# Optimization experiments

Measured on AMD Instinct MI355X. Metric: run time of the kernel, lower is better.

The kernel has to match this reference:

```python
import jax, jax.numpy as jnp
import numpy as np

B, S, HID = 2, 2048, 2048
H, D, KV = 16, 128, 4          # heads, head_dim, kv heads
REP = H // KV                  # GQA repeat factor
THETA = 10000.0


def setup_inputs() -> dict:
    key = jax.random.key(0)
    ks = jax.random.split(key, 12)
    query = jax.random.normal(ks[0], (B, S, HID), jnp.float32)
    k_in = jax.random.normal(ks[1], (B, S, HID), jnp.float32)
    v_in = jax.random.normal(ks[2], (B, S, HID), jnp.float32)
    # additive causal mask: 0 on/below diag, -10000 above
    causal = jnp.tril(jnp.ones((S, S), jnp.float32))
    mask = jnp.broadcast_to((1.0 - causal) * -10000.0, (B, 1, S, S))
    # rotary tables (cos/sin of freqs_cis), shape [S, D//2]
    inv_freq = 1.0 / (THETA ** (jnp.arange(0, D, 2, dtype=jnp.float32) / D))
    ang = jnp.outer(jnp.arange(S, dtype=jnp.float32), inv_freq)
    freqs_cos, freqs_sin = jnp.cos(ang), jnp.sin(ang)
    sd = 0.02
    Wq = jax.random.normal(ks[3], (HID, H * D), jnp.float32) * sd
    bq = jnp.zeros((H * D,), jnp.float32)
    Wk = jax.random.normal(ks[4], (HID, KV * D), jnp.float32) * sd
    bk = jnp.zeros((KV * D,), jnp.float32)
    Wv = jax.random.normal(ks[5], (HID, KV * D), jnp.float32) * sd
    bv = jnp.zeros((KV * D,), jnp.float32)
    Wo = jax.random.normal(ks[6], (H * D, HID), jnp.float32) * sd
    bo = jnp.zeros((HID,), jnp.float32)
    return {"query": query, "key": k_in, "value": v_in, "mask": mask,
            "freqs_cos": freqs_cos, "freqs_sin": freqs_sin,
            "Wq": Wq, "bq": bq, "Wk": Wk, "bk": bk,
            "Wv": Wv, "bv": bv, "Wo": Wo, "bo": bo}


def _rope(x, cos, sin):
    # x: [B,S,h,D]; pairs adjacent dims as complex (view_as_complex)
    xr = x.reshape(*x.shape[:-1], D // 2, 2)
    xe, xo = xr[..., 0], xr[..., 1]
    c = cos[None, :, None, :]
    s = sin[None, :, None, :]
    re = xe * c - xo * s
    im = xe * s + xo * c
    return jnp.stack([re, im], axis=-1).reshape(x.shape)


def reference(query, key, value, mask, freqs_cos, freqs_sin,
              Wq, bq, Wk, bk, Wv, bv, Wo, bo):
    q = (query @ Wq + bq).reshape(B, S, H, D)
    k = (key @ Wk + bk).reshape(B, S, KV, D)
    v = (value @ Wv + bv).reshape(B, S, KV, D)
    # repeat_kv: torch.repeat_interleave along head dim
    k = jnp.repeat(k, REP, axis=2)
    v = jnpp_repeat = jnp.repeat(v, REP, axis=2)
    q = _rope(q, freqs_cos, freqs_sin)
    k = _rope(k, freqs_cos, freqs_sin)
    q = q.transpose(0, 2, 1, 3)  # [B,H,S,D]
    k = k.transpose(0, 2, 1, 3)
    v = v.transpose(0, 2, 1, 3)
    scores = jnp.einsum('bhqd,bhkd->bhqk', q, k) / jnp.sqrt(jnp.float32(D))
    scores = scores + mask
    probs = jax.nn.softmax(scores, axis=-1)
    ctx = jnp.einsum('bhqk,bhkd->bhqd', probs, v)
    ctx = ctx.transpose(0, 2, 1, 3).reshape(B, S, H * D)
    return ctx @ Wo + bo
```

## Files before the change

kernel.cpp:

```cpp
#include <hip/hip_runtime.h>
#include <stdint.h>

#define BB 2
#define SS 2048
#define HID 2048
#define NH 16
#define DD 128
#define NKV 4

typedef unsigned short u16;
typedef __attribute__((ext_vector_type(8))) short short8;
typedef __attribute__((ext_vector_type(4))) float f32x4;

#if __has_builtin(__builtin_amdgcn_exp2f)
#define EXP2(x) __builtin_amdgcn_exp2f(x)
#else
#define EXP2(x) exp2f(x)
#endif

__device__ __forceinline__ u16 f2bf(float x) {
    union { float f; unsigned u; } v; v.f = x;
    unsigned u = v.u;
    return (u16)((u + 0x7FFFu + ((u >> 16) & 1u)) >> 16);
}

__device__ __forceinline__ void async_lds16(const void* g, void* l) {
    __builtin_amdgcn_global_load_lds(
        (const __attribute__((address_space(1))) void*)(uintptr_t)g,
        (__attribute__((address_space(3))) void*)(uintptr_t)l,
        16, 0, 0);
}

__global__ __launch_bounds__(256) void k_prep(const float* __restrict__ query,
                                              const float* __restrict__ key,
                                              const float* __restrict__ value,
                                              const float* __restrict__ Wq,
                                              const float* __restrict__ Wk,
                                              const float* __restrict__ Wv,
                                              const float* __restrict__ Wo,
                                              u16* __restrict__ qbf,
                                              u16* __restrict__ kbf,
                                              u16* __restrict__ vbf,
                                              u16* __restrict__ Wt,
                                              u16* __restrict__ Wot) {
    __shared__ float tile[32][33];
    int x = blockIdx.x;
    if (x < 24576) {
        const float* in; u16* out;
        if (x < 8192)       { in = query; out = qbf; }
        else if (x < 16384) { in = key;   out = kbf; x -= 8192; }
        else                { in = value; out = vbf; x -= 16384; }
        const int i = x * 256 + threadIdx.x;
        float4 v = ((const float4*)in)[i];
        uint2 o;
        o.x = (unsigned)f2bf(v.x) | ((unsigned)f2bf(v.y) << 16);
        o.y = (unsigned)f2bf(v.z) | ((unsigned)f2bf(v.w) << 16);
        ((uint2*)out)[i] = o;
        return;
    }
    const int v_ = x - 24576;
    const int ty = v_ / 160;
    const int xt = v_ - ty * 160;
    const float* src; u16* dst; int N, n0;
    if (xt < 64)      { src = Wq; dst = Wt;                          N = 2048; n0 = xt * 32; }
    else if (xt < 80) { src = Wk; dst = Wt + (size_t)2048 * 2048;    N = 512;  n0 = (xt - 64) * 32; }
    else if (xt < 96) { src = Wv; dst = Wt + (size_t)2560 * 2048;    N = 512;  n0 = (xt - 80) * 32; }
    else              { src = Wo; dst = Wot;                         N = 2048; n0 = (xt - 96) * 32; }
    const int k0 = ty * 32;
    const int c = threadIdx.x & 31, r = threadIdx.x >> 5;
#pragma unroll
    for (int i = 0; i < 32; i += 8)
        tile[r + i][c] = src[(size_t)(k0 + r + i) * N + n0 + c];
    __syncthreads();
#pragma unroll
    for (int i = 0; i < 32; i += 8)
        dst[(size_t)(n0 + r + i) * 2048 + k0 + c] = f2bf(tile[c][r + i]);
}

__global__ __launch_bounds__(256) void k_gemm_qkv(const u16* __restrict__ qbf,
                                                  const u16* __restrict__ kbf,
                                                  const u16* __restrict__ vbf,
                                                  const u16* __restrict__ Wt,
                                                  const float* __restrict__ bq,
                                                  const float* __restrict__ bk,
                                                  const float* __restrict__ bv,
                                                  const float* __restrict__ fc,
                                                  const float* __restrict__ fs,
                                                  u16* __restrict__ qro,
                                                  u16* __restrict__ kro,
                                                  u16* __restrict__ vtr) {
    __shared__ char smem[32768];
    u16* As = (u16*)smem;
    u16* Bs = (u16*)(smem + 16384);
    float* Ep = (float*)smem;

    const int tid = threadIdx.x;
    const int lane = tid & 63, wave = tid >> 6;
    const int bn = blockIdx.x;
    const int bm = blockIdx.y * 128;
    const u16* A = (bn < 16) ? qbf : (bn < 20) ? kbf : vbf;

    const int srow = wave * 8 + (lane >> 3);
    const int c0 = ((lane & 7) ^ (lane >> 3)) * 8;
    const u16* gA = A  + (size_t)(bm + srow) * 2048 + c0;
    const u16* gB = Wt + (size_t)(bn * 128 + srow) * 2048 + c0;

    const int r = lane & 15, q4 = lane >> 4;
    const int wm = (wave & 1) * 64, wn = (wave >> 1) * 64;

    int aoff[4][2], boff[4][2];
#pragma unroll
    for (int i = 0; i < 4; i++) {
        const int ar = wm + i * 16 + r;
        const int pa = q4 ^ (ar & 7);
        aoff[i][0] = ar * 64 + pa * 8;
        aoff[i][1] = ar * 64 + (pa ^ 4) * 8;
        const int br = wn + i * 16 + r;
        const int pb = q4 ^ (br & 7);
        boff[i][0] = br * 64 + pb * 8;
        boff[i][1] = br * 64 + (pb ^ 4) * 8;
    }

    f32x4 acc[4][4] = {};

    for (int kb = 0; kb < 2048; kb += 64) {
        async_lds16(gA,                       As + wave * 512);
        async_lds16(gA + (size_t)32 * 2048,   As + 2048 + wave * 512);
        async_lds16(gA + (size_t)64 * 2048,   As + 4096 + wave * 512);
        async_lds16(gA + (size_t)96 * 2048,   As + 6144 + wave * 512);
        async_lds16(gB,                       Bs + wave * 512);
        async_lds16(gB + (size_t)32 * 2048,   Bs + 2048 + wave * 512);
        async_lds16(gB + (size_t)64 * 2048,   Bs + 4096 + wave * 512);
        async_lds16(gB + (size_t)96 * 2048,   Bs + 6144 + wave * 512);
        gA += 64; gB += 64;
        __syncthreads();

#pragma unroll
        for (int kk = 0; kk < 2; kk++) {
            short8 av[4], bv_[4];
#pragma unroll
            for (int i = 0; i < 4; i++) av[i] = *(const short8*)(As + aoff[i][kk]);
#pragma unroll
            for (int j = 0; j < 4; j++) bv_[j] = *(const short8*)(Bs + boff[j][kk]);
#pragma unroll
            for (int i = 0; i < 4; i++)
#pragma unroll
                for (int j = 0; j < 4; j++)
                    acc[i][j] = __builtin_amdgcn_mfma_f32_16x16x32_bf16(av[i], bv_[j], acc[i][j], 0, 0, 0);
        }
        __syncthreads();
    }

    if (bn < 20) {
        const bool isQ = (bn < 16);
        const float qsc = isQ ? 0.08838834764831845f * 1.4426950408889634f : 1.0f;
        const float* bias = isQ ? bq : bk;
        const int head = isQ ? bn : (bn - 16);
        u16* base = isQ ? qro : kro;
        const int nheads = isQ ? NH : NKV;

        float* ep = Ep + wave * 1280;
        const int rowg = bm + wm + lane;
        const int s = rowg & 2047, bidx = rowg >> 11;
        const float* fcp0 = fc + s * 64;
        const float* fsp0 = fs + s * 64;

#pragma unroll
        for (int j = 0; j < 4; j++) {
            const float bcol = bias[head * 128 + wn + j * 16 + r];
#pragma unroll
            for (int i = 0; i < 4; i++)
#pragma unroll
                for (int g = 0; g < 4; g++)
                    ep[(i * 16 + q4 * 4 + g) * 20 + r] = acc[i][j][g] + bcol;
            float4 x0 = *(float4*)(ep + lane * 20 + 0);
            float4 x1 = *(float4*)(ep + lane * 20 + 4);
            float4 x2 = *(float4*)(ep + lane * 20 + 8);
            float4 x3 = *(float4*)(ep + lane * 20 + 12);
            const int d0 = wn + j * 16;
            const int ii0 = d0 >> 1;
            float4 ca = *(const float4*)(fcp0 + ii0);
            float4 cb = *(const float4*)(fcp0 + ii0 + 4);
            float4 sa = *(const float4*)(fsp0 + ii0);
            float4 sb = *(const float4*)(fsp0 + ii0 + 4);
            float o[16];
            o[0]  = (x0.x * ca.x - x0.y * sa.x) * qsc;  o[1]  = (x0.x * sa.x + x0.y * ca.x) * qsc;
            o[2]  = (x0.z * ca.y - x0.w * sa.y) * qsc;  o[3]  = (x0.z * sa.y + x0.w * ca.y) * qsc;
            o[4]  = (x1.x * ca.z - x1.y * sa.z) * qsc;  o[5]  = (x1.x * sa.z + x1.y * ca.z) * qsc;
            o[6]  = (x1.z * ca.w - x1.w * sa.w) * qsc;  o[7]  = (x1.z * sa.w + x1.w * ca.w) * qsc;
            o[8]  = (x2.x * cb.x - x2.y * sb.x) * qsc;  o[9]  = (x2.x * sb.x + x2.y * cb.x) * qsc;
            o[10] = (x2.z * cb.y - x2.w * sb.y) * qsc;  o[11] = (x2.z * sb.y + x2.w * cb.y) * qsc;
            o[12] = (x3.x * cb.z - x3.y * sb.z) * qsc;  o[13] = (x3.x * sb.z + x3.y * cb.z) * qsc;
            o[14] = (x3.z * cb.w - x3.w * sb.w) * qsc;  o[15] = (x3.z * sb.w + x3.w * cb.w) * qsc;
            unsigned w0 = (unsigned)f2bf(o[0])  | ((unsigned)f2bf(o[1])  << 16);
            unsigned w1 = (unsigned)f2bf(o[2])  | ((unsigned)f2bf(o[3])  << 16);
            unsigned w2 = (unsigned)f2bf(o[4])  | ((unsigned)f2bf(o[5])  << 16);
            unsigned w3 = (unsigned)f2bf(o[6])  | ((unsigned)f2bf(o[7])  << 16);
            unsigned w4 = (unsigned)f2bf(o[8])  | ((unsigned)f2bf(o[9])  << 16);
            unsigned w5 = (unsigned)f2bf(o[10]) | ((unsigned)f2bf(o[11]) << 16);
            unsigned w6 = (unsigned)f2bf(o[12]) | ((unsigned)f2bf(o[13]) << 16);
            unsigned w7 = (unsigned)f2bf(o[14]) | ((unsigned)f2bf(o[15]) << 16);
            u16* dst = base + (((size_t)(bidx * nheads + head) * SS + s) << 7) + d0;
            *(uint4*)dst = make_uint4(w0, w1, w2, w3);
            *(uint4*)(dst + 8) = make_uint4(w4, w5, w6, w7);
        }
    } else {
#pragma unroll
        for (int j = 0; j < 4; j++) {
            const int col = bn * 128 + wn + j * 16 + r - 2560;
            const int d = col & 127, kv = col >> 7;
            const float bb = bv[col];
#pragma unroll
            for (int i = 0; i < 4; i++) {
                const int row0 = bm + wm + i * 16 + q4 * 4;
                const int s0 = row0 & 2047, b = row0 >> 11;
                uint2 o;
                o.x = (unsigned)f2bf(acc[i][j][0] + bb) | ((unsigned)f2bf(acc[i][j][1] + bb) << 16);
                o.y = (unsigned)f2bf(acc[i][j][2] + bb) | ((unsigned)f2bf(acc[i][j][3] + bb) << 16);
                *(uint2*)(vtr + ((size_t)(b * NKV + kv) * DD + d) * SS + s0) = o;
            }
        }
    }
}

__global__ __launch_bounds__(256) void k_gemm_bt(const u16* __restrict__ A,
                                                 const u16* __restrict__ Bt,
                                                 const float* __restrict__ bias,
                                                 float* __restrict__ C,
                                                 int M, int N, int K) {
    __shared__ char smem[32768];
    u16* As = (u16*)smem;
    u16* Bs = (u16*)(smem + 16384);

    const int tid = threadIdx.x;
    const int lane = tid & 63, wave = tid >> 6;
    const int bm = blockIdx.y * 128, bn = blockIdx.x * 128;

    const int srow = wave * 8 + (lane >> 3);
    const int c0 = ((lane & 7) ^ (lane >> 3)) * 8;
    const u16* gA = A  + (size_t)(bm + srow) * K + c0;
    const u16* gB = Bt + (size_t)(bn + srow) * K + c0;

    const int r = lane & 15, q4 = lane >> 4;
    const int wm = (wave & 1) * 64, wn = (wave >> 1) * 64;

    int aoff[4][2], boff[4][2];
#pragma unroll
    for (int i = 0; i < 4; i++) {
        const int ar = wm + i * 16 + r;
        const int pa = q4 ^ (ar & 7);
        aoff[i][0] = ar * 64 + pa * 8;
        aoff[i][1] = ar * 64 + (pa ^ 4) * 8;
        const int br = wn + i * 16 + r;
        const int pb = q4 ^ (br & 7);
        boff[i][0] = br * 64 + pb * 8;
        boff[i][1] = br * 64 + (pb ^ 4) * 8;
    }

    f32x4 acc[4][4] = {};

    for (int kb = 0; kb < K; kb += 64) {
        async_lds16(gA,                    As + wave * 512);
        async_lds16(gA + (size_t)32 * K,   As + 2048 + wave * 512);
        async_lds16(gA + (size_t)64 * K,   As + 4096 + wave * 512);
        async_lds16(gA + (size_t)96 * K,   As + 6144 + wave * 512);
        async_lds16(gB,                    Bs + wave * 512);
        async_lds16(gB + (size_t)32 * K,   Bs + 2048 + wave * 512);
        async_lds16(gB + (size_t)64 * K,   Bs + 4096 + wave * 512);
        async_lds16(gB + (size_t)96 * K,   Bs + 6144 + wave * 512);
        gA += 64; gB += 64;
        __syncthreads();

#pragma unroll
        for (int kk = 0; kk < 2; kk++) {
            short8 av[4], bv_[4];
#pragma unroll
            for (int i = 0; i < 4; i++) av[i] = *(const short8*)(As + aoff[i][kk]);
#pragma unroll
            for (int j = 0; j < 4; j++) bv_[j] = *(const short8*)(Bs + boff[j][kk]);
#pragma unroll
            for (int i = 0; i < 4; i++)
#pragma unroll
                for (int j = 0; j < 4; j++)
                    acc[i][j] = __builtin_amdgcn_mfma_f32_16x16x32_bf16(av[i], bv_[j], acc[i][j], 0, 0, 0);
        }
        __syncthreads();
    }

#pragma unroll
    for (int j = 0; j < 4; j++) {
        const int col = bn + wn + j * 16 + r;
        const float bb = bias[col];
#pragma unroll
        for (int i = 0; i < 4; i++) {
            const int row = bm + wm + i * 16 + q4 * 4;
#pragma unroll
            for (int g = 0; g < 4; g++)
                C[(size_t)(row + g) * N + col] = acc[i][j][g] + bb;
        }
    }
}

__global__ __launch_bounds__(256) void k_attn(const u16* __restrict__ Q,
                                              const u16* __restrict__ K_,
                                              const u16* __restrict__ V_,
                                              u16* __restrict__ Ctx) {
    __shared__ u16 Ks[32 * 128];
    __shared__ u16 Vs[128 * 32];
    __shared__ u16 Pb[4 * 32 * 40];

    const int tid = threadIdx.x;
    const int lane = tid & 63, wave = tid >> 6;
    const int bh = blockIdx.x;
    const int b = bh >> 4, h = bh & 15;
    const int kvh = (b << 2) | (h >> 2);
    const int qb = (gridDim.y - 1 - blockIdx.y) * 128;
    const int qcol = lane & 15, q4 = lane >> 4;
    const int qw = qb + wave * 32;

    const u16* Qg = Q + ((size_t)bh * SS + qw + qcol) * DD;
    short8 qfr[2][4];
#pragma unroll
    for (int qi = 0; qi < 2; qi++)
#pragma unroll
        for (int c = 0; c < 4; c++)
            qfr[qi][c] = *(const short8*)(Qg + qi * 16 * DD + c * 32 + q4 * 8);

    const u16* Kg = K_ + (size_t)kvh * SS * DD;
    const u16* Vg = V_ + (size_t)kvh * DD * SS;

    const int krow = tid >> 4;
    const int kchunk = (tid & 15) ^ (krow & 7);
    const int vd = tid >> 2;
    const int vchunk = (tid & 3) ^ ((vd >> 1) & 3);

    f32x4 lacc[2] = {};
    f32x4 oacc[2][8] = {};

    const short8 ones = {0x3F80, 0x3F80, 0x3F80, 0x3F80, 0x3F80, 0x3F80, 0x3F80, 0x3F80};
    u16* pb = Pb + wave * 1280;
    unsigned* pb32 = (unsigned*)pb;

    for (int kb = 0; kb < qb + 128; kb += 32) {
        async_lds16(Kg + (size_t)(kb + krow) * DD + kchunk * 8,       Ks + wave * 512);
        async_lds16(Kg + (size_t)(kb + 16 + krow) * DD + kchunk * 8,  Ks + 2048 + wave * 512);
        async_lds16(Vg + (size_t)vd * SS + kb + vchunk * 8,           Vs + wave * 512);
        async_lds16(Vg + (size_t)(vd + 64) * SS + kb + vchunk * 8,    Vs + 2048 + wave * 512);
        __syncthreads();

        if (kb <= qw + 31) {
            f32x4 sc[2][2] = {};
#pragma unroll
            for (int kt = 0; kt < 2; kt++) {
                const int kr = kt * 16 + qcol;
#pragma unroll
                for (int c = 0; c < 4; c++) {
                    short8 kf = *(const short8*)(Ks + kr * 128 + (((c * 4 + q4) ^ (kr & 7)) << 3));
                    sc[kt][0] = __builtin_amdgcn_mfma_f32_16x16x32_bf16(kf, qfr[0][c], sc[kt][0], 0, 0, 0);
                    sc[kt][1] = __builtin_amdgcn_mfma_f32_16x16x32_bf16(kf, qfr[1][c], sc[kt][1], 0, 0, 0);
                }
            }

            if (kb + 32 > qw) {
#pragma unroll
                for (int kt = 0; kt < 2; kt++)
#pragma unroll
                    for (int qi = 0; qi < 2; qi++)
#pragma unroll
                        for (int g = 0; g < 4; g++) {
                            const int key = kb + kt * 16 + q4 * 4 + g;
                            if (key > qw + qi * 16 + qcol) sc[kt][qi][g] = -1e30f;
                        }
            }

            const unsigned sel = 0x07060302u;
#pragma unroll
            for (int qi = 0; qi < 2; qi++) {
                float p0 = EXP2(sc[0][qi][0]), p1 = EXP2(sc[0][qi][1]);
                float p2 = EXP2(sc[0][qi][2]), p3 = EXP2(sc[0][qi][3]);
                float p4 = EXP2(sc[1][qi][0]), p5 = EXP2(sc[1][qi][1]);
                float p6 = EXP2(sc[1][qi][2]), p7 = EXP2(sc[1][qi][3]);
                unsigned pk0 = __builtin_amdgcn_perm(__float_as_uint(p1), __float_as_uint(p0), sel);
                unsigned pk1 = __builtin_amdgcn_perm(__float_as_uint(p3), __float_as_uint(p2), sel);
                unsigned pk2 = __builtin_amdgcn_perm(__float_as_uint(p5), __float_as_uint(p4), sel);
                unsigned pk3 = __builtin_amdgcn_perm(__float_as_uint(p7), __float_as_uint(p6), sel);
                const int row = qi * 16 + qcol;
                *(uint2*)(pb32 + row * 20 + 2 * q4)     = make_uint2(pk0, pk1);
                *(uint2*)(pb32 + row * 20 + 8 + 2 * q4) = make_uint2(pk2, pk3);
            }

            short8 pf0 = *(const short8*)(pb + qcol * 40 + q4 * 8);
            short8 pf1 = *(const short8*)(pb + (16 + qcol) * 40 + q4 * 8);

            lacc[0] = __builtin_amdgcn_mfma_f32_16x16x32_bf16(ones, pf0, lacc[0], 0, 0, 0);
            lacc[1] = __builtin_amdgcn_mfma_f32_16x16x32_bf16(ones, pf1, lacc[1], 0, 0, 0);
#pragma unroll
            for (int dt = 0; dt < 8; dt++) {
                const int vr = dt * 16 + qcol;
                short8 vfr = *(const short8*)(Vs + vr * 32 + ((q4 ^ ((vr >> 1) & 3)) << 3));
                oacc[0][dt] = __builtin_amdgcn_mfma_f32_16x16x32_bf16(vfr, pf0, oacc[0][dt], 0, 0, 0);
                oacc[1][dt] = __builtin_amdgcn_mfma_f32_16x16x32_bf16(vfr, pf1, oacc[1][dt], 0, 0, 0);
            }
        }
        __syncthreads();
    }

#pragma unroll
    for (int qi = 0; qi < 2; qi++) {
        const float inv = 1.0f / lacc[qi][0];
        u16* outp = Ctx + ((size_t)b * SS + qw + qi * 16 + qcol) * (NH * DD) + h * DD;
#pragma unroll
        for (int dt = 0; dt < 8; dt++) {
            unsigned lo = (unsigned)f2bf(oacc[qi][dt][0] * inv) | ((unsigned)f2bf(oacc[qi][dt][1] * inv) << 16);
            unsigned hi = (unsigned)f2bf(oacc[qi][dt][2] * inv) | ((unsigned)f2bf(oacc[qi][dt][3] * inv) << 16);
            *(uint2*)(outp + dt * 16 + q4 * 4) = make_uint2(lo, hi);
        }
    }
}

extern "C" void kernel_launch(void* const* d_in, const int* in_sizes, int n_in,
                              void* d_out, int out_size, void* d_ws, size_t ws_size,
                              hipStream_t stream) {
    const float* query = (const float*)d_in[0];
    const float* key   = (const float*)d_in[1];
    const float* value = (const float*)d_in[2];
    const float* fc    = (const float*)d_in[4];
    const float* fs    = (const float*)d_in[5];
    const float* Wq    = (const float*)d_in[6];
    const float* bq    = (const float*)d_in[7];
    const float* Wk    = (const float*)d_in[8];
    const float* bk    = (const float*)d_in[9];
    const float* Wv    = (const float*)d_in[10];
    const float* bv    = (const float*)d_in[11];
    const float* Wo    = (const float*)d_in[12];
    const float* bo    = (const float*)d_in[13];
    float* out = (float*)d_out;

    char* w = (char*)d_ws;
    u16* qbf = (u16*)(w);
    u16* kbf = (u16*)(w + 16777216);
    u16* vbf = (u16*)(w + 33554432);
    u16* Wt  = (u16*)(w + 50331648);
    u16* Wot = (u16*)(w + 62914560);
    u16* qro = (u16*)(w + 71303168);
    u16* kro = (u16*)(w + 88080384);
    u16* vtr = (u16*)(w + 92274688);
    u16* ctx = (u16*)(w + 96468992);

    k_prep<<<34816, 256, 0, stream>>>(query, key, value, Wq, Wk, Wv, Wo,
                                      qbf, kbf, vbf, Wt, Wot);
    k_gemm_qkv<<<dim3(24, 32), 256, 0, stream>>>(qbf, kbf, vbf, Wt, bq, bk, bv,
                                                 fc, fs, qro, kro, vtr);
    k_attn<<<dim3(32, 16), 256, 0, stream>>>(qro, kro, vtr, ctx);
    k_gemm_bt<<<dim3(16, 32), 256, 0, stream>>>(ctx, Wot, bo, out, 4096, 2048, 2048);
}
```

Before: 400.5 us.

## Double-buffer GEMM and attention K/V tiles with async prefetch and block swizzle

Adds a shared double-buffered GEMM main loop that prefetches the next K-tile into LDS while computing MFMAs on the current one. The QKV and output GEMMs share this loop, and their block indices are remapped so blocks running together reuse cached tiles. The attention kernel now stages 64-key K/V tiles into double buffers and prefetches the next tile during compute, with s_setprio raised around the MFMA sections. The goal is to hide global-load latency and cut barriers, at the cost of twice the LDS (64KB per GEMM block), which may lower occupancy.

Result: faster. 364.6 us (-9.0%).

```diff
diff --git a/kernel.cpp b/kernel.cpp
--- a/kernel.cpp
+++ b/kernel.cpp
@@ -77,27 +77,91 @@
         dst[(size_t)(n0 + r + i) * 2048 + k0 + c] = f2bf(tile[c][r + i]);
 }
 
-__global__ __launch_bounds__(256) void k_gemm_qkv(const u16* __restrict__ qbf,
-                                                  const u16* __restrict__ kbf,
-                                                  const u16* __restrict__ vbf,
-                                                  const u16* __restrict__ Wt,
-                                                  const float* __restrict__ bq,
-                                                  const float* __restrict__ bk,
-                                                  const float* __restrict__ bv,
-                                                  const float* __restrict__ fc,
-                                                  const float* __restrict__ fs,
-                                                  u16* __restrict__ qro,
-                                                  u16* __restrict__ kro,
-                                                  u16* __restrict__ vtr) {
-    __shared__ char smem[32768];
+__device__ __forceinline__ void gemm128_loop(const u16* __restrict__ gA,
+                                             const u16* __restrict__ gB,
+                                             const int K, char* smem,
+                                             const int wave, const int lane,
+                                             f32x4 (&acc)[4][4]) {
+    const int r = lane & 15, q4 = lane >> 4;
+    const int wm = (wave & 1) * 64, wn = (wave >> 1) * 64;
     u16* As = (u16*)smem;
-    u16* Bs = (u16*)(smem + 16384);
-    float* Ep = (float*)smem;
-
+    u16* Bs = (u16*)(smem + 32768);
+
+    int aoff[4], boff[4];
+#pragma unroll
+    for (int i = 0; i < 4; i++) {
+        const int ar = wm + i * 16 + r;
+        aoff[i] = ar * 64 + ((q4 ^ (ar & 7)) << 3);
+        const int br = wn + i * 16 + r;
+        boff[i] = br * 64 + ((q4 ^ (br & 7)) << 3);
+    }
+
+    const int nt = K >> 6;
+
+#define STG128(buf, T) do {                                                                 \
+        _Pragma("unroll")                                                                   \
+        for (int i_ = 0; i_ < 4; i_++) {                                                    \
+            async_lds16(gA + (size_t)(i_ * 32) * K + (size_t)(T) * 64,                      \
+                        smem + (buf) * 16384 + (i_ * 32 + wave * 8) * 128);                 \
+            async_lds16(gB + (size_t)(i_ * 32) * K + (size_t)(T) * 64,                      \
+                        smem + 32768 + (buf) * 16384 + (i_ * 32 + wave * 8) * 128);         \
+        }                                                                                   \
+    } while (0)
+
+    STG128(0, 0);
+
+    for (int t = 0; t < nt; t++) {
+        const int cur = t & 1;
+        asm volatile("s_waitcnt vmcnt(0)" ::: "memory");
+        __syncthreads();
+        if (t + 1 < nt) STG128(cur ^ 1, t + 1);
+
+        const u16* Ab = As + cur * 8192;
+        const u16* Bb = Bs + cur * 8192;
+        short8 Af[4][2], Bf[4][2];
+#pragma unroll
+        for (int i = 0; i < 4; i++) {
+            Af[i][0] = *(const short8*)(Ab + aoff[i]);
+            Af[i][1] = *(const short8*)(Ab + (aoff[i] ^ 32));
+            Bf[i][0] = *(const short8*)(Bb + boff[i]);
+            Bf[i][1] = *(const short8*)(Bb + (boff[i] ^ 32));
+        }
+        __builtin_amdgcn_s_setprio(1);
+#pragma unroll
+        for (int kk = 0; kk < 2; kk++)
+#pragma unroll
+            for (int i = 0; i < 4; i++)
+#pragma unroll
+                for (int j = 0; j < 4; j++)
+                    acc[i][j] = __builtin_amdgcn_mfma_f32_16x16x32_bf16(Af[i][kk], Bf[j][kk], acc[i][j], 0, 0, 0);
+        __builtin_amdgcn_s_setprio(0);
+    }
+#undef STG128
+}
+
+__global__ __launch_bounds__(256, 2) void k_gemm_qkv(const u16* __restrict__ qbf,
+                                                     const u16* __restrict__ kbf,
+                                                     const u16* __restrict__ vbf,
+                                                     const u16* __restrict__ Wt,
+                                                     const float* __restrict__ bq,
+                                                     const float* __restrict__ bk,
+                                                     const float* __restrict__ bv,
+                                                     const float* __restrict__ fc,
+                                                     const float* __restrict__ fs,
+                                                     u16* __restrict__ qro,
+                                                     u16* __restrict__ kro,
+                                                     u16* __restrict__ vtr) {
+    __shared__ char smem[65536];
     const int tid = threadIdx.x;
     const int lane = tid & 63, wave = tid >> 6;
-    const int bn = blockIdx.x;
-    const int bm = blockIdx.y * 128;
+    const int r = lane & 15, q4 = lane >> 4;
+    const int wm = (wave & 1) * 64, wn = (wave >> 1) * 64;
+
+    const int linear = blockIdx.y * 24 + blockIdx.x;
+    const int nb = (linear & 7) * 96 + (linear >> 3);
+    const int bn = nb % 24;
+    const int bm = (nb / 24) * 128;
+
     const u16* A = (bn < 16) ? qbf : (bn < 20) ? kbf : vbf;
 
     const int srow = wave * 8 + (lane >> 3);
@@ -105,52 +169,12 @@
     const u16* gA = A  + (size_t)(bm + srow) * 2048 + c0;
     const u16* gB = Wt + (size_t)(bn * 128 + srow) * 2048 + c0;
 
-    const int r = lane & 15, q4 = lane >> 4;
-    const int wm = (wave & 1) * 64, wn = (wave >> 1) * 64;
-
-    int aoff[4][2], boff[4][2];
-#pragma unroll
-    for (int i = 0; i < 4; i++) {
-        const int ar = wm + i * 16 + r;
-        const int pa = q4 ^ (ar & 7);
-        aoff[i][0] = ar * 64 + pa * 8;
-        aoff[i][1] = ar * 64 + (pa ^ 4) * 8;
-        const int br = wn + i * 16 + r;
-        const int pb = q4 ^ (br & 7);
-        boff[i][0] = br * 64 + pb * 8;
-        boff[i][1] = br * 64 + (pb ^ 4) * 8;
-    }
-
     f32x4 acc[4][4] = {};
-
-    for (int kb = 0; kb < 2048; kb += 64) {
-        async_lds16(gA,                       As + wave * 512);
-        async_lds16(gA + (size_t)32 * 2048,   As + 2048 + wave * 512);
-        async_lds16(gA + (size_t)64 * 2048,   As + 4096 + wave * 512);
-        async_lds16(gA + (size_t)96 * 2048,   As + 6144 + wave * 512);
-        async_lds16(gB,                       Bs + wave * 512);
-        async_lds16(gB + (size_t)32 * 2048,   Bs + 2048 + wave * 512);
-        async_lds16(gB + (size_t)64 * 2048,   Bs + 4096 + wave * 512);
-        async_lds16(gB + (size_t)96 * 2048,   Bs + 6144 + wave * 512);
-        gA += 64; gB += 64;
-        __syncthreads();
-
-#pragma unroll
-        for (int kk = 0; kk < 2; kk++) {
-            short8 av[4], bv_[4];
-#pragma unroll
-            for (int i = 0; i < 4; i++) av[i] = *(const short8*)(As + aoff[i][kk]);
-#pragma unroll
-            for (int j = 0; j < 4; j++) bv_[j] = *(const short8*)(Bs + boff[j][kk]);
-#pragma unroll
-            for (int i = 0; i < 4; i++)
-#pragma unroll
-                for (int j = 0; j < 4; j++)
-                    acc[i][j] = __builtin_amdgcn_mfma_f32_16x16x32_bf16(av[i], bv_[j], acc[i][j], 0, 0, 0);
-        }
-        __syncthreads();
-    }
-
+    gemm128_loop(gA, gB, 2048, smem, wave, lane, acc);
+
+    __syncthreads();
+
+    float* Ep = (float*)smem;
     if (bn < 20) {
         const bool isQ = (bn < 16);
         const float qsc = isQ ? 0.08838834764831845f * 1.4426950408889634f : 1.0f;
@@ -223,77 +247,37 @@
     }
 }
 
-__global__ __launch_bounds__(256) void k_gemm_bt(const u16* __restrict__ A,
-                                                 const u16* __restrict__ Bt,
-                                                 const float* __restrict__ bias,
-                                                 float* __restrict__ C,
-                                                 int M, int N, int K) {
-    __shared__ char smem[32768];
-    u16* As = (u16*)smem;
-    u16* Bs = (u16*)(smem + 16384);
-
+__global__ __launch_bounds__(256, 2) void k_gemm_bt(const u16* __restrict__ A,
+                                                    const u16* __restrict__ Bt,
+                                                    const float* __restrict__ bias,
+                                                    float* __restrict__ C,
+                                                    int M, int N, int K) {
+    __shared__ char smem[65536];
     const int tid = threadIdx.x;
     const int lane = tid & 63, wave = tid >> 6;
-    const int bm = blockIdx.y * 128, bn = blockIdx.x * 128;
+    const int r = lane & 15, q4 = lane >> 4;
+    const int wm = (wave & 1) * 64, wn = (wave >> 1) * 64;
+
+    const int linear = blockIdx.y * 16 + blockIdx.x;
+    const int nb = (linear & 7) * 64 + (linear >> 3);
+    const int bn0 = (nb & 15) * 128;
+    const int bm0 = (nb >> 4) * 128;
 
     const int srow = wave * 8 + (lane >> 3);
     const int c0 = ((lane & 7) ^ (lane >> 3)) * 8;
-    const u16* gA = A  + (size_t)(bm + srow) * K + c0;
-    const u16* gB = Bt + (size_t)(bn + srow) * K + c0;
-
-    const int r = lane & 15, q4 = lane >> 4;
-    const int wm = (wave & 1) * 64, wn = (wave >> 1) * 64;
-
-    int aoff[4][2], boff[4][2];
-#pragma unroll
-    for (int i = 0; i < 4; i++) {
-        const int ar = wm + i * 16 + r;
-        const int pa = q4 ^ (ar & 7);
-        aoff[i][0] = ar * 64 + pa * 8;
-        aoff[i][1] = ar * 64 + (pa ^ 4) * 8;
-        const int br = wn + i * 16 + r;
-        const int pb = q4 ^ (br & 7);
-        boff[i][0] = br * 64 + pb * 8;
-        boff[i][1] = br * 64 + (pb ^ 4) * 8;
-    }
+    const u16* gA = A  + (size_t)(bm0 + srow) * K + c0;
+    const u16* gB = Bt + (size_t)(bn0 + srow) * K + c0;
 
     f32x4 acc[4][4] = {};
-
-    for (int kb = 0; kb < K; kb += 64) {
-        async_lds16(gA,                    As + wave * 512);
-        async_lds16(gA + (size_t)32 * K,   As + 2048 + wave * 512);
-        async_lds16(gA + (size_t)64 * K,   As + 4096 + wave * 512);
-        async_lds16(gA + (size_t)96 * K,   As + 6144 + wave * 512);
-        async_lds16(gB,                    Bs + wave * 512);
-        async_lds16(gB + (size_t)32 * K,   Bs + 2048 + wave * 512);
-        async_lds16(gB + (size_t)64 * K,   Bs + 4096 + wave * 512);
-        async_lds16(gB + (size_t)96 * K,   Bs + 6144 + wave * 512);
-        gA += 64; gB += 64;
-        __syncthreads();
-
-#pragma unroll
-        for (int kk = 0; kk < 2; kk++) {
-            short8 av[4], bv_[4];
-#pragma unroll
-            for (int i = 0; i < 4; i++) av[i] = *(const short8*)(As + aoff[i][kk]);
-#pragma unroll
-            for (int j = 0; j < 4; j++) bv_[j] = *(const short8*)(Bs + boff[j][kk]);
-#pragma unroll
-            for (int i = 0; i < 4; i++)
-#pragma unroll
-                for (int j = 0; j < 4; j++)
-                    acc[i][j] = __builtin_amdgcn_mfma_f32_16x16x32_bf16(av[i], bv_[j], acc[i][j], 0, 0, 0);
-        }
-        __syncthreads();
-    }
+    gemm128_loop(gA, gB, K, smem, wave, lane, acc);
 
 #pragma unroll
     for (int j = 0; j < 4; j++) {
-        const int col = bn + wn + j * 16 + r;
+        const int col = bn0 + wn + j * 16 + r;
         const float bb = bias[col];
 #pragma unroll
         for (int i = 0; i < 4; i++) {
-            const int row = bm + wm + i * 16 + q4 * 4;
+            const int row = bm0 + wm + i * 16 + q4 * 4;
 #pragma unroll
             for (int g = 0; g < 4; g++)
                 C[(size_t)(row + g) * N + col] = acc[i][j][g] + bb;
@@ -305,9 +289,9 @@
                                               const u16* __restrict__ K_,
                                               const u16* __restrict__ V_,
                                               u16* __restrict__ Ctx) {
-    __shared__ u16 Ks[32 * 128];
-    __shared__ u16 Vs[128 * 32];
-    __shared__ u16 Pb[4 * 32 * 40];
+    __shared__ u16 Ks[2][64 * 128];
+    __shared__ u16 Vs[2][2 * 128 * 32];
+    __shared__ u16 Pb[4][32 * 40];
 
     const int tid = threadIdx.x;
     const int lane = tid & 63, wave = tid >> 6;
@@ -334,76 +318,103 @@
     const int vd = tid >> 2;
     const int vchunk = (tid & 3) ^ ((vd >> 1) & 3);
 
+    const int nt = (qb + 128) >> 6;
+    const int kmax = (nt - 1) * 64;
+
     f32x4 lacc[2] = {};
     f32x4 oacc[2][8] = {};
 
     const short8 ones = {0x3F80, 0x3F80, 0x3F80, 0x3F80, 0x3F80, 0x3F80, 0x3F80, 0x3F80};
-    u16* pb = Pb + wave * 1280;
+    u16* pb = &Pb[wave][0];
     unsigned* pb32 = (unsigned*)pb;
 
-    for (int kb = 0; kb < qb + 128; kb += 32) {
-        async_lds16(Kg + (size_t)(kb + krow) * DD + kchunk * 8,       Ks + wave * 512);
-        async_lds16(Kg + (size_t)(kb + 16 + krow) * DD + kchunk * 8,  Ks + 2048 + wave * 512);
-        async_lds16(Vg + (size_t)vd * SS + kb + vchunk * 8,           Vs + wave * 512);
-        async_lds16(Vg + (size_t)(vd + 64) * SS + kb + vchunk * 8,    Vs + 2048 + wave * 512);
-        __syncthreads();
-
-        if (kb <= qw + 31) {
-            f32x4 sc[2][2] = {};
-#pragma unroll
-            for (int kt = 0; kt < 2; kt++) {
-                const int kr = kt * 16 + qcol;
-#pragma unroll
-                for (int c = 0; c < 4; c++) {
-                    short8 kf = *(const short8*)(Ks + kr * 128 + (((c * 4 + q4) ^ (kr & 7)) << 3));
-                    sc[kt][0] = __builtin_amdgcn_mfma_f32_16x16x32_bf16(kf, qfr[0][c], sc[kt][0], 0, 0, 0);
-                    sc[kt][1] = __builtin_amdgcn_mfma_f32_16x16x32_bf16(kf, qfr[1][c], sc[kt][1], 0, 0, 0);
+#define STAGE_KV(T, BUF) do {                                                                   \
+        const int kb_ = min((T) * 64, kmax);                                                    \
+        async_lds16(Kg + (size_t)(kb_ + krow) * DD + kchunk * 8,        &Ks[BUF][0] + wave * 512);        \
+        async_lds16(Kg + (size_t)(kb_ + 16 + krow) * DD + kchunk * 8,   &Ks[BUF][0] + 2048 + wave * 512); \
+        async_lds16(Kg + (size_t)(kb_ + 32 + krow) * DD + kchunk * 8,   &Ks[BUF][0] + 4096 + wave * 512); \
+        async_lds16(Kg + (size_t)(kb_ + 48 + krow) * DD + kchunk * 8,   &Ks[BUF][0] + 6144 + wave * 512); \
+        async_lds16(Vg + (size_t)vd * SS + kb_ + vchunk * 8,            &Vs[BUF][0] + wave * 512);        \
+        async_lds16(Vg + (size_t)vd * SS + kb_ + 32 + vchunk * 8,       &Vs[BUF][0] + 4096 + wave * 512); \
+        async_lds16(Vg + (size_t)(vd + 64) * SS + kb_ + vchunk * 8,     &Vs[BUF][0] + 2048 + wave * 512); \
+        async_lds16(Vg + (size_t)(vd + 64) * SS + kb_ + 32 + vchunk * 8,&Vs[BUF][0] + 6144 + wave * 512); \
+    } while (0)
+
+    STAGE_KV(0, 0);
+
+    for (int t = 0; t < nt; t++) {
+        const int kb = t * 64;
+        const int cur = t & 1;
+        asm volatile("s_waitcnt vmcnt(0)\n\ts_barrier" ::: "memory");
+        if (t + 1 < nt) STAGE_KV(t + 1, cur ^ 1);
+
+#pragma unroll
+        for (int hh = 0; hh < 2; hh++) {
+            const int kbh = kb + hh * 32;
+            if (kbh <= qw + 31) {
+                const u16* Ksc = &Ks[cur][hh * 32 * 128];
+                const u16* Vsc = &Vs[cur][hh * 4096];
+
+                f32x4 sc[2][2] = {};
+                __builtin_amdgcn_s_setprio(1);
+#pragma unroll
+                for (int kt = 0; kt < 2; kt++) {
+                    const int kr = kt * 16 + qcol;
+#pragma unroll
+                    for (int c = 0; c < 4; c++) {
+                        short8 kf = *(const short8*)(Ksc + kr * 128 + (((c * 4 + q4) ^ (kr & 7)) << 3));
+                        sc[kt][0] = __builtin_amdgcn_mfma_f32_16x16x32_bf16(kf, qfr[0][c], sc[kt][0], 0, 0, 0);
+                        sc[kt][1] = __builtin_amdgcn_mfma_f32_16x16x32_bf16(kf, qfr[1][c], sc[kt][1], 0, 0, 0);
+                    }
                 }
+                __builtin_amdgcn_s_setprio(0);
+
+                if (kbh + 32 > qw) {
+#pragma unroll
+                    for (int kt = 0; kt < 2; kt++)
+#pragma unroll
+                        for (int qi = 0; qi < 2; qi++)
+#pragma unroll
+                            for (int g = 0; g < 4; g++) {
+                                const int key = kbh + kt * 16 + q4 * 4 + g;
+                                if (key > qw + qi * 16 + qcol) sc[kt][qi][g] = -1e30f;
+                            }
+                }
+
+                const unsigned sel = 0x07060302u;
+#pragma unroll
+                for (int qi = 0; qi < 2; qi++) {
+                    float p0 = EXP2(sc[0][qi][0]), p1 = EXP2(sc[0][qi][1]);
+                    float p2 = EXP2(sc[0][qi][2]), p3 = EXP2(sc[0][qi][3]);
+                    float p4 = EXP2(sc[1][qi][0]), p5 = EXP2(sc[1][qi][1]);
+                    float p6 = EXP2(sc[1][qi][2]), p7 = EXP2(sc[1][qi][3]);
+                    unsigned pk0 = __builtin_amdgcn_perm(__float_as_uint(p1), __float_as_uint(p0), sel);
+                    unsigned pk1 = __builtin_amdgcn_perm(__float_as_uint(p3), __float_as_uint(p2), sel);
+                    unsigned pk2 = __builtin_amdgcn_perm(__float_as_uint(p5), __float_as_uint(p4), sel);
+                    unsigned pk3 = __builtin_amdgcn_perm(__float_as_uint(p7), __float_as_uint(p6), sel);
+                    const int row = qi * 16 + qcol;
+                    *(uint2*)(pb32 + row * 20 + 2 * q4)     = make_uint2(pk0, pk1);
+                    *(uint2*)(pb32 + row * 20 + 8 + 2 * q4) = make_uint2(pk2, pk3);
+                }
+
+                short8 pf0 = *(const short8*)(pb + qcol * 40 + q4 * 8);
+                short8 pf1 = *(const short8*)(pb + (16 + qcol) * 40 + q4 * 8);
+
+                __builtin_amdgcn_s_setprio(1);
+                lacc[0] = __builtin_amdgcn_mfma_f32_16x16x32_bf16(ones, pf0, lacc[0], 0, 0, 0);
+                lacc[1] = __builtin_amdgcn_mfma_f32_16x16x32_bf16(ones, pf1, lacc[1], 0, 0, 0);
+#pragma unroll
+                for (int dt = 0; dt < 8; dt++) {
+                    const int vr = dt * 16 + qcol;
+                    short8 vfr = *(const short8*)(Vsc + vr * 32 + ((q4 ^ ((vr >> 1) & 3)) << 3));
+                    oacc[0][dt] = __builtin_amdgcn_mfma_f32_16x16x32_bf16(vfr, pf0, oacc[0][dt], 0, 0, 0);
+                    oacc[1][dt] = __builtin_amdgcn_mfma_f32_16x16x32_bf16(vfr, pf1, oacc[1][dt], 0, 0, 0);
+                }
+                __builtin_amdgcn_s_setprio(0);
             }
-
-            if (kb + 32 > qw) {
-#pragma unroll
-                for (int kt = 0; kt < 2; kt++)
-#pragma unroll
-                    for (int qi = 0; qi < 2; qi++)
-#pragma unroll
-                        for (int g = 0; g < 4; g++) {
-                            const int key = kb + kt * 16 + q4 * 4 + g;
-                            if (key > qw + qi * 16 + qcol) sc[kt][qi][g] = -1e30f;
-                        }
-            }
-
-            const unsigned sel = 0x07060302u;
-#pragma unroll
-            for (int qi = 0; qi < 2; qi++) {
-                float p0 = EXP2(sc[0][qi][0]), p1 = EXP2(sc[0][qi][1]);
-                float p2 = EXP2(sc[0][qi][2]), p3 = EXP2(sc[0][qi][3]);
-                float p4 = EXP2(sc[1][qi][0]), p5 = EXP2(sc[1][qi][1]);
-                float p6 = EXP2(sc[1][qi][2]), p7 = EXP2(sc[1][qi][3]);
-                unsigned pk0 = __builtin_amdgcn_perm(__float_as_uint(p1), __float_as_uint(p0), sel);
-                unsigned pk1 = __builtin_amdgcn_perm(__float_as_uint(p3), __float_as_uint(p2), sel);
-                unsigned pk2 = __builtin_amdgcn_perm(__float_as_uint(p5), __float_as_uint(p4), sel);
-                unsigned pk3 = __builtin_amdgcn_perm(__float_as_uint(p7), __float_as_uint(p6), sel);
-                const int row = qi * 16 + qcol;
-                *(uint2*)(pb32 + row * 20 + 2 * q4)     = make_uint2(pk0, pk1);
-                *(uint2*)(pb32 + row * 20 + 8 + 2 * q4) = make_uint2(pk2, pk3);
-            }
-
-            short8 pf0 = *(const short8*)(pb + qcol * 40 + q4 * 8);
-            short8 pf1 = *(const short8*)(pb + (16 + qcol) * 40 + q4 * 8);
-
-            lacc[0] = __builtin_amdgcn_mfma_f32_16x16x32_bf16(ones, pf0, lacc[0], 0, 0, 0);
-            lacc[1] = __builtin_amdgcn_mfma_f32_16x16x32_bf16(ones, pf1, lacc[1], 0, 0, 0);
-#pragma unroll
-            for (int dt = 0; dt < 8; dt++) {
-                const int vr = dt * 16 + qcol;
-                short8 vfr = *(const short8*)(Vs + vr * 32 + ((q4 ^ ((vr >> 1) & 3)) << 3));
-                oacc[0][dt] = __builtin_amdgcn_mfma_f32_16x16x32_bf16(vfr, pf0, oacc[0][dt], 0, 0, 0);
-                oacc[1][dt] = __builtin_amdgcn_mfma_f32_16x16x32_bf16(vfr, pf1, oacc[1][dt], 0, 0, 0);
-            }
-        }
-        __syncthreads();
-    }
+        }
+    }
+#undef STAGE_KV
 
 #pragma unroll
     for (int qi = 0; qi < 2; qi++) {
```
